# Kernel optimization log

Hardware: AMD Instinct MI355X
Metric: run time of the kernel (lower is better)

Reference implementation:

```python
import jax, jax.numpy as jnp
import numpy as np

N_NEURONS = 256
WINDOW = 20


def setup_inputs() -> dict:
    key = jax.random.key(0)
    k1, k2, k3 = jax.random.split(key, 3)
    basis = jax.random.uniform(k1, (WINDOW,), dtype=jnp.float32)  # spike-history basis
    # Linear(n_neurons, n_neurons) params, torch default-ish scale
    scale = 1.0 / np.sqrt(N_NEURONS)
    weight = jax.random.normal(k2, (N_NEURONS, N_NEURONS), dtype=jnp.float32) * scale
    bias = jax.random.normal(k3, (N_NEURONS,), dtype=jnp.float32) * scale
    return {
        "basis": basis,
        "weight": weight,
        "bias": bias,
        "n_time_bins": 1024,
        "n_samples": 64,
    }


def reference(basis, weight, bias, n_time_bins, n_samples):
    """POGLM.sample(): sequential basis-conv + linear + sigmoid + Poisson draw.

    Returns stacked (spikes, convolved_spikes, firing_rates), each [S, T, N],
    as a single [3, S, T, N] array.
    """
    W = basis.shape[0]
    N = weight.shape[0]
    flipped_basis = basis[::-1]  # torch.flip(basis, (0,))
    keys = jax.random.split(jax.random.key(1), n_time_bins)
    buf0 = jnp.zeros((n_samples, W, N), dtype=jnp.float32)  # last W spike frames

    def step(buf, k):
        # flipped_basis @ spikes[:, t:t+W, :]  -> [S, N]
        conv = jnp.einsum('w,swn->sn', flipped_basis, buf)
        rates = jax.nn.sigmoid(conv @ weight.T + bias)
        spk = jax.random.poisson(k, rates).astype(rates.dtype)
        buf = jnp.concatenate([buf[:, 1:, :], spk[:, None, :]], axis=1)
        return buf, (spk, conv, rates)

    _, (spikes, conv, rates) = jax.lax.scan(step, buf0, keys)
    # scan stacks over time: [T, S, N] -> [S, T, N]
    out = jnp.stack([spikes, conv, rates], axis=0)  # [3, T, S, N]
    return out.transpose(0, 2, 1, 3)  # [3, S, T, N]
```

## Files before the change

### kernel.cpp

```cpp
#include <hip/hip_runtime.h>
#include <stdint.h>
#include <math.h>

#define THREEFRY_PARTITIONABLE 1
#define BITS32_XOR 1
#define VSL_FMA 0
#define CONV_FMA 0
#define RAW_BARRIER 1
#define POISSON_BATCH 4
#define NT_STORES 1
#define J_PRE 8

#define T_BINS 1024
#define N_SAMP 64
#define N_NEUR 256
#define J_MAX 32
#define LANES (N_SAMP * N_NEUR)

#define SUB_BYTES   (T_BINS * 2 * J_MAX * 4)
#define HIST_OFF    SUB_BYTES
#define HIST_BYTES  (20 * LANES * 4)
#define STBL_OFF    (HIST_OFF + HIST_BYTES)

static __device__ __forceinline__ float fmul_s(float a, float b) {
#pragma clang fp contract(off)
  return a * b;
}
static __device__ __forceinline__ float fadd_s(float a, float b) {
#pragma clang fp contract(off)
  return a + b;
}
static __device__ __forceinline__ float fsub_s(float a, float b) {
#pragma clang fp contract(off)
  return a - b;
}

#if VSL_FMA
#define MULADD(a, b, c) __builtin_fmaf((a), (b), (c))
#else
#define MULADD(a, b, c) fadd_s(fmul_s((a), (b)), (c))
#endif

static __device__ __forceinline__ uint32_t rotl(uint32_t v, uint32_t d) {
  return (v << d) | (v >> (32u - d));
}
static __device__ __forceinline__ void threefry2x32(uint32_t k0, uint32_t k1,
                                                    uint32_t x0, uint32_t x1,
                                                    uint32_t& o0, uint32_t& o1) {
  const uint32_t k2 = k0 ^ k1 ^ 0x1BD11BDAu;
  x0 += k0; x1 += k1;
#define TF_RD(r) { x0 += x1; x1 = rotl(x1, r); x1 ^= x0; }
  TF_RD(13u) TF_RD(15u) TF_RD(26u) TF_RD(6u)
  x0 += k1; x1 += k2 + 1u;
  TF_RD(17u) TF_RD(29u) TF_RD(16u) TF_RD(24u)
  x0 += k2; x1 += k0 + 2u;
  TF_RD(13u) TF_RD(15u) TF_RD(26u) TF_RD(6u)
  x0 += k0; x1 += k1 + 3u;
  TF_RD(17u) TF_RD(29u) TF_RD(16u) TF_RD(24u)
  x0 += k1; x1 += k2 + 4u;
  TF_RD(13u) TF_RD(15u) TF_RD(26u) TF_RD(6u)
  x0 += k2; x1 += k0 + 5u;
#undef TF_RD
  o0 = x0; o1 = x1;
}

static __device__ __forceinline__ float xla_expf(float input) {
  float x = fminf(input, 88.3762626647950f);
  x = fmaxf(x, -88.3762626647949f);
  float fx = floorf(MULADD(x, 1.44269504088896341f, 0.5f));
  float tmp = fmul_s(0.693359375f, fx);
  float z = fmul_s(-2.12194440e-4f, fx);
  x = fsub_s(x, tmp);
  x = fsub_s(x, z);
  z = fmul_s(x, x);
  float y = MULADD(x, 1.9875691500e-4f, 1.3981999507e-3f);
  y = MULADD(y, x, 8.3334519073e-3f);
  y = MULADD(y, x, 4.1665795894e-2f);
  y = MULADD(y, x, 1.6666665459e-1f);
  y = MULADD(y, x, 5.0000001201e-1f);
  y = MULADD(y, z, x);
  y = fadd_s(1.0f, y);
  int n = (int)fx;
  float p2n = __int_as_float((uint32_t)(n + 127) << 23);
  float res = fmul_s(y, p2n);
  return fmaxf(res, input);
}

static __device__ __forceinline__ float xla_logf(float u) {
  if (u == 0.0f) return -INFINITY;
  uint32_t b = __float_as_uint(u);
  float e = (float)((int)(b >> 23) - 127) + 1.0f;
  float m = __uint_as_float((b & 0x007fffffu) | 0x3f000000u);
  if (m < 0.707106781186547524f) {
    e = fsub_s(e, 1.0f);
    m = fadd_s(m, m);
  }
  m = fsub_s(m, 1.0f);
  float z = fmul_s(m, m);
  float y = MULADD(m, 7.0376836292e-2f, -1.1514610310e-1f);
  y = MULADD(y, m, 1.1676998740e-1f);
  y = MULADD(y, m, -1.2420140846e-1f);
  y = MULADD(y, m, 1.4249322787e-1f);
  y = MULADD(y, m, -1.6668057665e-1f);
  y = MULADD(y, m, 2.0000714765e-1f);
  y = MULADD(y, m, -2.4999993993e-1f);
  y = MULADD(y, m, 3.3333331174e-1f);
  y = fmul_s(y, m);
  y = fmul_s(y, z);
  y = MULADD(e, -2.12194440e-4f, y);
  y = MULADD(z, -0.5f, y);
  m = fadd_s(m, y);
  m = MULADD(e, 0.693359375f, m);
  return m;
}

__global__ void poglm_subkeys(uint32_t* __restrict__ sub) {
  int t = blockIdx.x * blockDim.x + threadIdx.x;
  if (t >= T_BINS) return;
  uint32_t kt0, kt1;
#if THREEFRY_PARTITIONABLE
  threefry2x32(0u, 1u, 0u, (uint32_t)t, kt0, kt1);
#else
  {
    uint32_t i0 = 2u * t, i1 = 2u * t + 1u, a0, a1, b0, b1;
    if (i0 < 1024u) { threefry2x32(0u, 1u, i0, i0 + 1024u, a0, a1); kt0 = a0; }
    else            { threefry2x32(0u, 1u, i0 - 1024u, i0, a0, a1); kt0 = a1; }
    if (i1 < 1024u) { threefry2x32(0u, 1u, i1, i1 + 1024u, b0, b1); kt1 = b0; }
    else            { threefry2x32(0u, 1u, i1 - 1024u, i1, b0, b1); kt1 = b1; }
  }
#endif
  uint32_t r0 = kt0, r1 = kt1;
  for (int j = 0; j < J_MAX; ++j) {
    uint32_t s0, s1, n0, n1;
#if THREEFRY_PARTITIONABLE
    threefry2x32(r0, r1, 0u, 1u, s0, s1);
    threefry2x32(r0, r1, 0u, 0u, n0, n1);
#else
    uint32_t p00, p01, p10, p11;
    threefry2x32(r0, r1, 0u, 2u, p00, p01);
    threefry2x32(r0, r1, 1u, 3u, p10, p11);
    n0 = p00; n1 = p10;
    s0 = p01; s1 = p11;
#endif
    sub[(size_t)t * (2 * J_MAX) + 2 * j + 0] = s0;
    sub[(size_t)t * (2 * J_MAX) + 2 * j + 1] = s1;
    r0 = n0; r1 = n1;
  }
}

__global__ __launch_bounds__(256)
void poglm_stable(const uint32_t* __restrict__ sub, float* __restrict__ S8,
                  int t0) {
  const int g   = blockIdx.x * 256 + threadIdx.x;
  const int tt  = t0 + g / LANES;
  const int ln  = g % LANES;
  float S = 0.0f;
  float v[J_PRE];
#pragma unroll
  for (int j = 0; j < J_PRE; ++j) {
    const uint32_t k0 = sub[(size_t)tt * (2 * J_MAX) + 2 * j];
    const uint32_t k1 = sub[(size_t)tt * (2 * J_MAX) + 2 * j + 1];
    uint32_t o0, o1;
    threefry2x32(k0, k1, 0u, (uint32_t)ln, o0, o1);
#if BITS32_XOR
    const uint32_t bits = o0 ^ o1;
#else
    const uint32_t bits = o1;
#endif
    const float u = __uint_as_float((bits >> 9) | 0x3f800000u) - 1.0f;
    S = fadd_s(S, xla_logf(u));
    v[j] = S;
  }
  float4* dst = reinterpret_cast<float4*>(S8 + (size_t)g * J_PRE);
  dst[0] = make_float4(v[0], v[1], v[2], v[3]);
  dst[1] = make_float4(v[4], v[5], v[6], v[7]);
}

#define FOR64(M) \
  M(0) M(1) M(2) M(3) M(4) M(5) M(6) M(7) M(8) M(9) M(10) M(11) M(12) M(13) \
  M(14) M(15) M(16) M(17) M(18) M(19) M(20) M(21) M(22) M(23) M(24) M(25)   \
  M(26) M(27) M(28) M(29) M(30) M(31) M(32) M(33) M(34) M(35) M(36) M(37)   \
  M(38) M(39) M(40) M(41) M(42) M(43) M(44) M(45) M(46) M(47) M(48) M(49)   \
  M(50) M(51) M(52) M(53) M(54) M(55) M(56) M(57) M(58) M(59) M(60) M(61)   \
  M(62) M(63)

#define WDECL(i) float wA##i, wB##i, wC##i, wD##i;

#define WLOADPIN(i)                                                          \
  { const float4 v_ = w4[i];                                                 \
    asm volatile("v_accvgpr_write_b32 %0, %1" : "=a"(wA##i) : "v"(v_.x));    \
    asm volatile("v_accvgpr_write_b32 %0, %1" : "=a"(wB##i) : "v"(v_.y));    \
    asm volatile("v_accvgpr_write_b32 %0, %1" : "=a"(wC##i) : "v"(v_.z));    \
    asm volatile("v_accvgpr_write_b32 %0, %1" : "=a"(wD##i) : "v"(v_.w)); }

#define LOADCV(u, i) const float4 cv##u = convbuf4[i];
#define AFMA(u, i)                                                           \
  { float wa_, wb_, wc_, wd_;                                                \
    asm volatile("v_accvgpr_read_b32 %0, %1" : "=v"(wa_) : "a"(wA##i));      \
    asm volatile("v_accvgpr_read_b32 %0, %1" : "=v"(wb_) : "a"(wB##i));      \
    asm volatile("v_accvgpr_read_b32 %0, %1" : "=v"(wc_) : "a"(wC##i));      \
    asm volatile("v_accvgpr_read_b32 %0, %1" : "=v"(wd_) : "a"(wD##i));      \
    zacc = __builtin_fmaf(cv##u.x, wa_, zacc);                               \
    zacc = __builtin_fmaf(cv##u.y, wb_, zacc);                               \
    zacc = __builtin_fmaf(cv##u.z, wc_, zacc);                               \
    zacc = __builtin_fmaf(cv##u.w, wd_, zacc); }

#define ZCHUNK(i0,i1,i2,i3,i4,i5,i6,i7)                                      \
  { LOADCV(0,i0) LOADCV(1,i1) LOADCV(2,i2) LOADCV(3,i3)                      \
    LOADCV(4,i4) LOADCV(5,i5) LOADCV(6,i6) LOADCV(7,i7)                      \
    AFMA(0,i0) AFMA(1,i1) AFMA(2,i2) AFMA(3,i3)                              \
    AFMA(4,i4) AFMA(5,i5) AFMA(6,i6) AFMA(7,i7) }

template <int MODE>
__global__ __launch_bounds__(256, 1)
void poglm_main(const float* __restrict__ basis, const float* __restrict__ weight,
                const float* __restrict__ bias, const uint32_t* __restrict__ sub,
                float* __restrict__ out, const float* __restrict__ S8,
                float* __restrict__ histws, int t0, int t1) {
  __shared__ alignas(16) float convb[2][N_NEUR];
  __shared__ uint32_t skb[2][2 * J_MAX];
  __shared__ float fb[20];

  const int s = blockIdx.x;
  const int n = threadIdx.x;

  if (n < 20) fb[n] = basis[19 - n];
  const float bias_n = bias[n];

  const float4* __restrict__ w4 =
      reinterpret_cast<const float4*>(weight + (size_t)n * N_NEUR);
  FOR64(WDECL)
  FOR64(WLOADPIN)

  const uint32_t idx = (uint32_t)(s * N_NEUR + n);

  float hist[20];
  if (t0 == 0) {
#pragma unroll
    for (int i = 0; i < 20; ++i) hist[i] = 0.0f;
  } else {
#pragma unroll
    for (int i = 0; i < 20; ++i) hist[i] = histws[i * LANES + idx];
  }

  const size_t plane = (size_t)N_SAMP * T_BINS * N_NEUR;
  float* __restrict__ out_spk = out + 0 * plane + (size_t)s * T_BINS * N_NEUR + n;
  float* __restrict__ out_cnv = out + 1 * plane + (size_t)s * T_BINS * N_NEUR + n;
  float* __restrict__ out_rte = out + 2 * plane + (size_t)s * T_BINS * N_NEUR + n;

  uint32_t skreg = 0;
  float4 sc0, sc1;
  if constexpr (MODE == 0) {
    if (n < 2 * J_MAX) skreg = sub[(size_t)t0 * (2 * J_MAX) + n];
  } else {
    const float4* p = reinterpret_cast<const float4*>(S8 + (size_t)idx * J_PRE);
    sc0 = p[0]; sc1 = p[1];
  }

  __syncthreads();

  for (int t = t0; t < t1; ++t) {
    const int buf = t & 1;
    float* __restrict__ convbuf = convb[buf];
    const float4* __restrict__ convbuf4 = reinterpret_cast<const float4*>(convbuf);

    float4 sn0, sn1;
    if constexpr (MODE == 0) {
      uint32_t* __restrict__ skbuf = skb[buf];
      if (n < 2 * J_MAX) {
        skbuf[n] = skreg;
        const int tn = (t + 1 < t1) ? t + 1 : t;
        skreg = sub[(size_t)tn * (2 * J_MAX) + n];
      }
    } else {
      const int tn = (t + 1 < t1) ? t + 1 : t;
      const float4* p = reinterpret_cast<const float4*>(
          S8 + ((size_t)(tn - t0) * LANES + idx) * J_PRE);
      sn0 = p[0]; sn1 = p[1];
    }

    float conv = 0.0f;
#pragma unroll
    for (int w = 0; w < 20; ++w) {
#if CONV_FMA
      conv = __builtin_fmaf(fb[w], hist[w], conv);
#else
      conv = fadd_s(conv, fmul_s(fb[w], hist[w]));
#endif
    }
    convbuf[n] = conv;

#if RAW_BARRIER
    asm volatile("s_waitcnt lgkmcnt(0)\n\ts_barrier" ::: "memory");
#else
    __syncthreads();
#endif

    float zacc = 0.0f;
    ZCHUNK(0,1,2,3,4,5,6,7)
    ZCHUNK(8,9,10,11,12,13,14,15)
    ZCHUNK(16,17,18,19,20,21,22,23)
    ZCHUNK(24,25,26,27,28,29,30,31)
    ZCHUNK(32,33,34,35,36,37,38,39)
    ZCHUNK(40,41,42,43,44,45,46,47)
    ZCHUNK(48,49,50,51,52,53,54,55)
    ZCHUNK(56,57,58,59,60,61,62,63)
    const float zb = fadd_s(zacc, bias_n);

    const float lam = 1.0f / fadd_s(1.0f, xla_expf(-zb));
    const float neg_lam = -lam;

    int r = 0;
    if constexpr (MODE == 1) {
      r = (sc0.x > neg_lam) + (sc0.y > neg_lam) + (sc0.z > neg_lam) +
          (sc0.w > neg_lam) + (sc1.x > neg_lam) + (sc1.y > neg_lam) +
          (sc1.z > neg_lam) + (sc1.w > neg_lam);
      if (sc1.w > neg_lam) {
        float S = sc1.w;
#pragma unroll 1
        for (int j = J_PRE; j < J_MAX; ++j) {
          const uint32_t k0 = sub[(size_t)t * (2 * J_MAX) + 2 * j];
          const uint32_t k1 = sub[(size_t)t * (2 * J_MAX) + 2 * j + 1];
          uint32_t o0, o1;
          threefry2x32(k0, k1, 0u, idx, o0, o1);
#if BITS32_XOR
          const uint32_t bits = o0 ^ o1;
#else
          const uint32_t bits = o1;
#endif
          const float u = __uint_as_float((bits >> 9) | 0x3f800000u) - 1.0f;
          S = fadd_s(S, xla_logf(u));
          if (S > neg_lam) ++r; else break;
        }
      }
    } else {
      uint32_t* __restrict__ skbuf = skb[buf];
      float S = 0.0f;
      bool done = false;
#pragma unroll 1
      for (int jb = 0; jb < J_MAX; jb += POISSON_BATCH) {
        float L[POISSON_BATCH];
#pragma unroll
        for (int q = 0; q < POISSON_BATCH; ++q) {
          const int j = jb + q;
          uint32_t o0, o1;
          threefry2x32(skbuf[2 * j], skbuf[2 * j + 1], 0u, idx, o0, o1);
#if BITS32_XOR
          const uint32_t bits = o0 ^ o1;
#else
          const uint32_t bits = o1;
#endif
          const float u = __uint_as_float((bits >> 9) | 0x3f800000u) - 1.0f;
          L[q] = xla_logf(u);
        }
#pragma unroll
        for (int q = 0; q < POISSON_BATCH; ++q) {
          if (!done) {
            S = fadd_s(S, L[q]);
            if (S > neg_lam) ++r; else done = true;
          }
        }
        if (__all(done)) break;
      }
    }
    const float spk = (float)r;

#pragma unroll
    for (int i = 0; i < 19; ++i) hist[i] = hist[i + 1];
    hist[19] = spk;

    const size_t off = (size_t)t * N_NEUR;
#if NT_STORES
    __builtin_nontemporal_store(spk,  out_spk + off);
    __builtin_nontemporal_store(conv, out_cnv + off);
    __builtin_nontemporal_store(lam,  out_rte + off);
#else
    out_spk[off] = spk;
    out_cnv[off] = conv;
    out_rte[off] = lam;
#endif
    if constexpr (MODE == 1) { sc0 = sn0; sc1 = sn1; }
#if !RAW_BARRIER
    __syncthreads();
#endif
  }

  if (t1 < T_BINS) {
#pragma unroll
    for (int i = 0; i < 20; ++i) histws[i * LANES + idx] = hist[i];
  }
}

extern "C" void kernel_launch(void* const* d_in, const int* in_sizes, int n_in,
                              void* d_out, int out_size, void* d_ws, size_t ws_size,
                              hipStream_t stream) {
  const float* basis  = (const float*)d_in[0];
  const float* weight = (const float*)d_in[1];
  const float* bias   = (const float*)d_in[2];
  float* out = (float*)d_out;
  char* ws = (char*)d_ws;
  uint32_t* sub = (uint32_t*)ws;
  float* histws = (float*)(ws + HIST_OFF);
  float* stbl = (float*)(ws + STBL_OFF);

  hipLaunchKernelGGL(poglm_subkeys, dim3((T_BINS + 255) / 256), dim3(256), 0,
                     stream, sub);

  int chunkT = 0;
  for (int c = T_BINS; c >= 64; c >>= 1) {
    const size_t bytes = (size_t)c * LANES * J_PRE * 4;
    if (STBL_OFF + bytes <= ws_size) { chunkT = c; break; }
  }

  if (chunkT == 0) {
    hipLaunchKernelGGL((poglm_main<0>), dim3(N_SAMP), dim3(256), 0,
                       stream, basis, weight, bias, sub, out,
                       (const float*)nullptr, histws, 0, T_BINS);
    return;
  }

  for (int t0 = 0; t0 < T_BINS; t0 += chunkT) {
    const int t1 = t0 + chunkT;
    hipLaunchKernelGGL(poglm_stable, dim3(chunkT * (LANES / 256)), dim3(256), 0,
                       stream, sub, stbl, t0);
    hipLaunchKernelGGL((poglm_main<1>), dim3(N_SAMP), dim3(256), 0,
                       stream, basis, weight, bias, sub, out,
                       (const float*)stbl, histws, t0, t1);
  }
}
```

Measured before the change: 2.169 ms.

## Overlap next-chunk Poisson table generation with sequential main kernel via fused grid

Merges the stable-table producer into the main recurrent kernel as extra blocks. While the 64 sequential sample blocks process chunk c, the remaining blocks precompute the log-uniform prefix table for chunk c+1 into a second double-buffered workspace. Only 64 blocks do the recurrent work, so the rest of the GPU was idle; this uses those CUs and hides the table-generation launches. It also reorders the AGPR reads ahead of the FMAs so they can be scheduled together, and changes how the chunk size is picked. The cost is twice the workspace, and the extra blocks may contend with the main blocks for memory bandwidth.

```diff
diff --git a/kernel.cpp b/kernel.cpp
--- a/kernel.cpp
+++ b/kernel.cpp
@@ -114,46 +114,9 @@
   return m;
 }
 
-__global__ void poglm_subkeys(uint32_t* __restrict__ sub) {
-  int t = blockIdx.x * blockDim.x + threadIdx.x;
-  if (t >= T_BINS) return;
-  uint32_t kt0, kt1;
-#if THREEFRY_PARTITIONABLE
-  threefry2x32(0u, 1u, 0u, (uint32_t)t, kt0, kt1);
-#else
-  {
-    uint32_t i0 = 2u * t, i1 = 2u * t + 1u, a0, a1, b0, b1;
-    if (i0 < 1024u) { threefry2x32(0u, 1u, i0, i0 + 1024u, a0, a1); kt0 = a0; }
-    else            { threefry2x32(0u, 1u, i0 - 1024u, i0, a0, a1); kt0 = a1; }
-    if (i1 < 1024u) { threefry2x32(0u, 1u, i1, i1 + 1024u, b0, b1); kt1 = b0; }
-    else            { threefry2x32(0u, 1u, i1 - 1024u, i1, b0, b1); kt1 = b1; }
-  }
-#endif
-  uint32_t r0 = kt0, r1 = kt1;
-  for (int j = 0; j < J_MAX; ++j) {
-    uint32_t s0, s1, n0, n1;
-#if THREEFRY_PARTITIONABLE
-    threefry2x32(r0, r1, 0u, 1u, s0, s1);
-    threefry2x32(r0, r1, 0u, 0u, n0, n1);
-#else
-    uint32_t p00, p01, p10, p11;
-    threefry2x32(r0, r1, 0u, 2u, p00, p01);
-    threefry2x32(r0, r1, 1u, 3u, p10, p11);
-    n0 = p00; n1 = p10;
-    s0 = p01; s1 = p11;
-#endif
-    sub[(size_t)t * (2 * J_MAX) + 2 * j + 0] = s0;
-    sub[(size_t)t * (2 * J_MAX) + 2 * j + 1] = s1;
-    r0 = n0; r1 = n1;
-  }
-}
-
-__global__ __launch_bounds__(256)
-void poglm_stable(const uint32_t* __restrict__ sub, float* __restrict__ S8,
-                  int t0) {
-  const int g   = blockIdx.x * 256 + threadIdx.x;
-  const int tt  = t0 + g / LANES;
-  const int ln  = g % LANES;
+static __device__ __forceinline__ void stable_body(
+    const uint32_t* __restrict__ sub, float* __restrict__ dst8,
+    int tt, int ln) {
   float S = 0.0f;
   float v[J_PRE];
 #pragma unroll
@@ -171,9 +134,52 @@
     S = fadd_s(S, xla_logf(u));
     v[j] = S;
   }
-  float4* dst = reinterpret_cast<float4*>(S8 + (size_t)g * J_PRE);
+  float4* dst = reinterpret_cast<float4*>(dst8);
   dst[0] = make_float4(v[0], v[1], v[2], v[3]);
   dst[1] = make_float4(v[4], v[5], v[6], v[7]);
+}
+
+__global__ void poglm_subkeys(uint32_t* __restrict__ sub) {
+  int t = blockIdx.x * blockDim.x + threadIdx.x;
+  if (t >= T_BINS) return;
+  uint32_t kt0, kt1;
+#if THREEFRY_PARTITIONABLE
+  threefry2x32(0u, 1u, 0u, (uint32_t)t, kt0, kt1);
+#else
+  {
+    uint32_t i0 = 2u * t, i1 = 2u * t + 1u, a0, a1, b0, b1;
+    if (i0 < 1024u) { threefry2x32(0u, 1u, i0, i0 + 1024u, a0, a1); kt0 = a0; }
+    else            { threefry2x32(0u, 1u, i0 - 1024u, i0, a0, a1); kt0 = a1; }
+    if (i1 < 1024u) { threefry2x32(0u, 1u, i1, i1 + 1024u, b0, b1); kt1 = b0; }
+    else            { threefry2x32(0u, 1u, i1 - 1024u, i1, b0, b1); kt1 = b1; }
+  }
+#endif
+  uint32_t r0 = kt0, r1 = kt1;
+  for (int j = 0; j < J_MAX; ++j) {
+    uint32_t s0, s1, n0, n1;
+#if THREEFRY_PARTITIONABLE
+    threefry2x32(r0, r1, 0u, 1u, s0, s1);
+    threefry2x32(r0, r1, 0u, 0u, n0, n1);
+#else
+    uint32_t p00, p01, p10, p11;
+    threefry2x32(r0, r1, 0u, 2u, p00, p01);
+    threefry2x32(r0, r1, 1u, 3u, p10, p11);
+    n0 = p00; n1 = p10;
+    s0 = p01; s1 = p11;
+#endif
+    sub[(size_t)t * (2 * J_MAX) + 2 * j + 0] = s0;
+    sub[(size_t)t * (2 * J_MAX) + 2 * j + 1] = s1;
+    r0 = n0; r1 = n1;
+  }
+}
+
+__global__ __launch_bounds__(256)
+void poglm_stable(const uint32_t* __restrict__ sub, float* __restrict__ S8,
+                  int t0) {
+  const int g  = blockIdx.x * 256 + threadIdx.x;
+  const int tt = t0 + g / LANES;
+  const int ln = g % LANES;
+  stable_body(sub, S8 + (size_t)g * J_PRE, tt, ln);
 }
 
 #define FOR64(M) \
@@ -194,29 +200,40 @@
     asm volatile("v_accvgpr_write_b32 %0, %1" : "=a"(wD##i) : "v"(v_.w)); }
 
 #define LOADCV(u, i) const float4 cv##u = convbuf4[i];
-#define AFMA(u, i)                                                           \
-  { float wa_, wb_, wc_, wd_;                                                \
-    asm volatile("v_accvgpr_read_b32 %0, %1" : "=v"(wa_) : "a"(wA##i));      \
-    asm volatile("v_accvgpr_read_b32 %0, %1" : "=v"(wb_) : "a"(wB##i));      \
-    asm volatile("v_accvgpr_read_b32 %0, %1" : "=v"(wc_) : "a"(wC##i));      \
-    asm volatile("v_accvgpr_read_b32 %0, %1" : "=v"(wd_) : "a"(wD##i));      \
-    zacc = __builtin_fmaf(cv##u.x, wa_, zacc);                               \
-    zacc = __builtin_fmaf(cv##u.y, wb_, zacc);                               \
-    zacc = __builtin_fmaf(cv##u.z, wc_, zacc);                               \
-    zacc = __builtin_fmaf(cv##u.w, wd_, zacc); }
+#define AREAD(u, i)                                                          \
+  float ta##u, tb##u, tc##u, td##u;                                          \
+  asm volatile("v_accvgpr_read_b32 %0, %1" : "=v"(ta##u) : "a"(wA##i));      \
+  asm volatile("v_accvgpr_read_b32 %0, %1" : "=v"(tb##u) : "a"(wB##i));      \
+  asm volatile("v_accvgpr_read_b32 %0, %1" : "=v"(tc##u) : "a"(wC##i));      \
+  asm volatile("v_accvgpr_read_b32 %0, %1" : "=v"(td##u) : "a"(wD##i));
+#define FMA4(u)                                                              \
+  zacc = __builtin_fmaf(cv##u.x, ta##u, zacc);                               \
+  zacc = __builtin_fmaf(cv##u.y, tb##u, zacc);                               \
+  zacc = __builtin_fmaf(cv##u.z, tc##u, zacc);                               \
+  zacc = __builtin_fmaf(cv##u.w, td##u, zacc);
 
 #define ZCHUNK(i0,i1,i2,i3,i4,i5,i6,i7)                                      \
   { LOADCV(0,i0) LOADCV(1,i1) LOADCV(2,i2) LOADCV(3,i3)                      \
     LOADCV(4,i4) LOADCV(5,i5) LOADCV(6,i6) LOADCV(7,i7)                      \
-    AFMA(0,i0) AFMA(1,i1) AFMA(2,i2) AFMA(3,i3)                              \
-    AFMA(4,i4) AFMA(5,i5) AFMA(6,i6) AFMA(7,i7) }
+    AREAD(0,i0) AREAD(1,i1) AREAD(2,i2) AREAD(3,i3)                          \
+    AREAD(4,i4) AREAD(5,i5) AREAD(6,i6) AREAD(7,i7)                          \
+    FMA4(0) FMA4(1) FMA4(2) FMA4(3) FMA4(4) FMA4(5) FMA4(6) FMA4(7) }
 
 template <int MODE>
 __global__ __launch_bounds__(256, 1)
-void poglm_main(const float* __restrict__ basis, const float* __restrict__ weight,
-                const float* __restrict__ bias, const uint32_t* __restrict__ sub,
-                float* __restrict__ out, const float* __restrict__ S8,
-                float* __restrict__ histws, int t0, int t1) {
+void poglm_fused(const float* __restrict__ basis, const float* __restrict__ weight,
+                 const float* __restrict__ bias, const uint32_t* __restrict__ sub,
+                 float* __restrict__ out, const float* __restrict__ S8_in,
+                 float* __restrict__ S8_out, int tb0,
+                 float* __restrict__ histws, int t0, int t1) {
+  if (MODE == 1 && blockIdx.x >= N_SAMP) {
+    const int g  = (blockIdx.x - N_SAMP) * 256 + threadIdx.x;
+    const int tt = tb0 + g / LANES;
+    const int ln = g % LANES;
+    stable_body(sub, S8_out + (size_t)g * J_PRE, tt, ln);
+    return;
+  }
+
   __shared__ alignas(16) float convb[2][N_NEUR];
   __shared__ uint32_t skb[2][2 * J_MAX];
   __shared__ float fb[20];
@@ -253,7 +270,7 @@
   if constexpr (MODE == 0) {
     if (n < 2 * J_MAX) skreg = sub[(size_t)t0 * (2 * J_MAX) + n];
   } else {
-    const float4* p = reinterpret_cast<const float4*>(S8 + (size_t)idx * J_PRE);
+    const float4* p = reinterpret_cast<const float4*>(S8_in + (size_t)idx * J_PRE);
     sc0 = p[0]; sc1 = p[1];
   }
 
@@ -275,7 +292,7 @@
     } else {
       const int tn = (t + 1 < t1) ? t + 1 : t;
       const float4* p = reinterpret_cast<const float4*>(
-          S8 + ((size_t)(tn - t0) * LANES + idx) * J_PRE);
+          S8_in + ((size_t)(tn - t0) * LANES + idx) * J_PRE);
       sn0 = p[0]; sn1 = p[1];
     }
 
@@ -401,30 +418,59 @@
   char* ws = (char*)d_ws;
   uint32_t* sub = (uint32_t*)ws;
   float* histws = (float*)(ws + HIST_OFF);
-  float* stbl = (float*)(ws + STBL_OFF);
 
   hipLaunchKernelGGL(poglm_subkeys, dim3((T_BINS + 255) / 256), dim3(256), 0,
                      stream, sub);
 
   int chunkT = 0;
-  for (int c = T_BINS; c >= 64; c >>= 1) {
-    const size_t bytes = (size_t)c * LANES * J_PRE * 4;
-    if (STBL_OFF + bytes <= ws_size) { chunkT = c; break; }
+  const int cand[4] = {256, 512, 128, 64};
+  for (int ci = 0; ci < 4; ++ci) {
+    const size_t bytes = (size_t)cand[ci] * LANES * J_PRE * 4;
+    if (STBL_OFF + 2 * bytes <= ws_size) { chunkT = cand[ci]; break; }
   }
 
   if (chunkT == 0) {
-    hipLaunchKernelGGL((poglm_main<0>), dim3(N_SAMP), dim3(256), 0,
+    int sc = 0;
+    for (int c = T_BINS; c >= 64; c >>= 1) {
+      const size_t bytes = (size_t)c * LANES * J_PRE * 4;
+      if (STBL_OFF + bytes <= ws_size) { sc = c; break; }
+    }
+    if (sc == 0) {
+      hipLaunchKernelGGL((poglm_fused<0>), dim3(N_SAMP), dim3(256), 0,
+                         stream, basis, weight, bias, sub, out,
+                         (const float*)nullptr, (float*)nullptr, 0,
+                         histws, 0, T_BINS);
+      return;
+    }
+    float* stbl = (float*)(ws + STBL_OFF);
+    for (int t0 = 0; t0 < T_BINS; t0 += sc) {
+      hipLaunchKernelGGL(poglm_stable, dim3(sc * (LANES / 256)), dim3(256), 0,
+                         stream, sub, stbl, t0);
+      hipLaunchKernelGGL((poglm_fused<1>), dim3(N_SAMP), dim3(256), 0,
+                         stream, basis, weight, bias, sub, out,
+                         (const float*)stbl, (float*)nullptr, 0,
+                         histws, t0, t0 + sc);
+    }
+    return;
+  }
+
+  const size_t stbl_bytes = (size_t)chunkT * LANES * J_PRE * 4;
+  float* stbl0 = (float*)(ws + STBL_OFF);
+  float* stbl1 = (float*)(ws + STBL_OFF + stbl_bytes);
+  const int nstb = chunkT * (LANES / 256);
+  const int nc = T_BINS / chunkT;
+
+  hipLaunchKernelGGL(poglm_stable, dim3(nstb), dim3(256), 0, stream,
+                     sub, stbl0, 0);
+
+  for (int c = 0; c < nc; ++c) {
+    const int t0 = c * chunkT, t1 = t0 + chunkT;
+    float* cur = (c & 1) ? stbl1 : stbl0;
+    float* nxt = (c & 1) ? stbl0 : stbl1;
+    const bool more = (c + 1 < nc);
+    hipLaunchKernelGGL((poglm_fused<1>),
+                       dim3(N_SAMP + (more ? nstb : 0)), dim3(256), 0,
                        stream, basis, weight, bias, sub, out,
-                       (const float*)nullptr, histws, 0, T_BINS);
-    return;
-  }
-
-  for (int t0 = 0; t0 < T_BINS; t0 += chunkT) {
-    const int t1 = t0 + chunkT;
-    hipLaunchKernelGGL(poglm_stable, dim3(chunkT * (LANES / 256)), dim3(256), 0,
-                       stream, sub, stbl, t0);
-    hipLaunchKernelGGL((poglm_main<1>), dim3(N_SAMP), dim3(256), 0,
-                       stream, basis, weight, bias, sub, out,
-                       (const float*)stbl, histws, t0, t1);
-  }
-}
+                       (const float*)cur, nxt, t1, histws, t0, t1);
+  }
+}
```

Measured after the change: 1.973 ms. 1.1x faster.
